# Optimization experiments

Hardware: AMD Instinct MI355X
Metric: run time of the kernel (lower is better)

The kernel has to match this reference:

```python
import jax, jax.numpy as jnp
import numpy as np
import math

H = 10  # hidden_dim (hardcoded in source)
D = 2   # data_dim (hardcoded in source)
T = 256
B = 2048

PARAM_SHAPES = {
    'fi_in_W': (D, H), 'fi_in_b': (H,), 'fi_h_W': (H, H), 'fi_h_b': (H,),
    'fi_mu_W': (H, H), 'fi_mu_b': (H,), 'fi_sg_W': (H, H), 'fi_sg_b': (H,),
    'inf_in_W': (D, H), 'inf_in_b': (H,), 'inf_j_W': (2 * H, H), 'inf_j_b': (H,),
    'inf_h_W': (H, H), 'inf_h_b': (H,), 'inf_mu_W': (H, H), 'inf_mu_b': (H,),
    'inf_sg_W': (H, H), 'inf_sg_b': (H,),
    'tr_h_W': (H, H), 'tr_h_b': (H,), 'tr_mu_W': (H, H), 'tr_mu_b': (H,),
    'tr_sg_W': (H, H), 'tr_sg_b': (H,),
    'gen_h1_W': (H, H), 'gen_h1_b': (H,), 'gen_h2_W': (H, H), 'gen_h2_b': (H,),
    'gen_mu_W': (H, D), 'gen_mu_b': (D,), 'gen_sg_W': (H, D), 'gen_sg_b': (D,),
}


def setup_inputs() -> dict:
    key = jax.random.key(0)
    names = list(PARAM_SHAPES)
    keys = jax.random.split(key, len(names) + 2)
    inp = {}
    inp['sequence'] = jax.random.normal(keys[0], (T, B, D), jnp.float32)
    inp['noise'] = jax.random.normal(keys[1], (T, B, H), jnp.float32)
    for n, k in zip(names, keys[2:]):
        inp[n] = 0.1 * jax.random.normal(k, PARAM_SHAPES[n], jnp.float32)
    # Transition sigma is tanh(.); shift its bias so sigma stays strictly positive
    # (a trained model would do the same; negative sigma makes the source's log(prod) NaN).
    inp['tr_sg_b'] = inp['tr_sg_b'] + 2.0
    return inp


def _forward(sequence, noise,
             fi_in_W, fi_in_b, fi_h_W, fi_h_b, fi_mu_W, fi_mu_b, fi_sg_W, fi_sg_b,
             inf_in_W, inf_in_b, inf_j_W, inf_j_b, inf_h_W, inf_h_b, inf_mu_W, inf_mu_b, inf_sg_W, inf_sg_b,
             tr_h_W, tr_h_b, tr_mu_W, tr_mu_b, tr_sg_W, tr_sg_b,
             gen_h1_W, gen_h1_b, gen_h2_W, gen_h2_b, gen_mu_W, gen_mu_b, gen_sg_W, gen_sg_b):

    def first_inf(x):
        h = jnp.tanh(x @ fi_in_W + fi_in_b)
        h = jnp.tanh(h @ fi_h_W + fi_h_b)
        return jnp.tanh(h @ fi_mu_W + fi_mu_b), jax.nn.sigmoid(h @ fi_sg_W + fi_sg_b) + 0.001

    def inference(x, z):
        e = jnp.tanh(x @ inf_in_W + inf_in_b)
        h = jnp.tanh(jnp.concatenate([e, z], -1) @ inf_j_W + inf_j_b)
        h = jnp.tanh(h @ inf_h_W + inf_h_b)
        return jnp.tanh(h @ inf_mu_W + inf_mu_b), jax.nn.sigmoid(h @ inf_sg_W + inf_sg_b) + 0.001

    def transition(z):
        h = jnp.tanh(z @ tr_h_W + tr_h_b)
        return jnp.tanh(h @ tr_mu_W + tr_mu_b), jnp.tanh(h @ tr_sg_W + tr_sg_b)

    def generator(z):
        h = jax.nn.relu(z @ gen_h1_W + gen_h1_b)
        h = jax.nn.relu(h @ gen_h2_W + gen_h2_b)
        return jax.nn.sigmoid(h @ gen_mu_W + gen_mu_b), jax.nn.sigmoid(h @ gen_sg_W + gen_sg_b)

    def kld(mu_q, sg_q, mu_p, sg_p):  # source GaussianKLD (treats sigma as variance)
        a = jnp.log(jnp.prod(sg_p, -1) / jnp.prod(sg_q, -1))
        b = jnp.sum(sg_q / sg_p, -1)
        c = jnp.sum((mu_p - mu_q) ** 2 / sg_p, -1)
        return 0.5 * (a + b + c - mu_q.shape[-1])

    def gll(mu, sg, target):  # source GaussianLL (note: log(pi), not 2*pi — faithful)
        a = jnp.log(jnp.prod(sg, -1))
        b = jnp.sum((target - mu) ** 2 / sg, -1)
        c = mu.shape[-1] * math.log(math.pi)
        return -0.5 * (a + b + c)

    # t = 0: first_inference against unit-Gaussian prior
    q_mu0, q_sg0 = first_inf(sequence[0])
    kl0 = kld(q_mu0, q_sg0, jnp.zeros_like(q_mu0), jnp.ones_like(q_sg0))
    z1 = q_mu0 + q_sg0 * noise[0]
    g_mu0, g_sg0 = generator(z1)
    loss0 = kl0 + gll(g_mu0, g_sg0, sequence[0])  # [B]

    def step(z_prev, xe):
        x_t, eps = xe
        pr_mu, pr_sg = transition(z_prev)
        q_mu, q_sg = inference(x_t, z_prev)
        kl_t = kld(q_mu, q_sg, pr_mu, pr_sg)
        z = q_mu + q_sg * eps
        m, s = generator(z)
        ll_t = gll(m, s, x_t)
        return z, (m, kl_t + ll_t)

    _, (gens_rest, step_losses) = jax.lax.scan(step, z1, (sequence[1:], noise[1:]))
    generations = jnp.concatenate([g_mu0[None], gens_rest], 0)  # [T, B, D]
    loss = loss0 + jnp.sum(step_losses, 0)                       # [B]
    return generations, -loss / sequence.shape[0]


def reference(sequence, noise,
              fi_in_W, fi_in_b, fi_h_W, fi_h_b, fi_mu_W, fi_mu_b, fi_sg_W, fi_sg_b,
              inf_in_W, inf_in_b, inf_j_W, inf_j_b, inf_h_W, inf_h_b, inf_mu_W, inf_mu_b, inf_sg_W, inf_sg_b,
              tr_h_W, tr_h_b, tr_mu_W, tr_mu_b, tr_sg_W, tr_sg_b,
              gen_h1_W, gen_h1_b, gen_h2_W, gen_h2_b, gen_mu_W, gen_mu_b, gen_sg_W, gen_sg_b):
    return _forward(sequence, noise,
                    fi_in_W, fi_in_b, fi_h_W, fi_h_b, fi_mu_W, fi_mu_b, fi_sg_W, fi_sg_b,
                    inf_in_W, inf_in_b, inf_j_W, inf_j_b, inf_h_W, inf_h_b, inf_mu_W, inf_mu_b, inf_sg_W, inf_sg_b,
                    tr_h_W, tr_h_b, tr_mu_W, tr_mu_b, tr_sg_W, tr_sg_b,
                    gen_h1_W, gen_h1_b, gen_h2_W, gen_h2_b, gen_mu_W, gen_mu_b, gen_sg_W, gen_sg_b)
```

## Files before the change

### kernel.cpp

```cpp
#include <hip/hip_runtime.h>
#include <math.h>

#define T_STEPS 256
#define BATCH   2048
#define HID     10

#define ZOFF   0
#define QMUOFF (T_STEPS*BATCH*HID)
#define QSGOFF (2*T_STEPS*BATCH*HID)
#define KLOFF  (3*T_STEPS*BATCH*HID)
#define LLOFF  (KLOFF + T_STEPS*BATCH)

#define S2P  2.8853900817779268f
#define SNP -1.4426950408889634f

typedef float v2f __attribute__((ext_vector_type(2)));

__device__ __forceinline__ float frcp(float x){ return __builtin_amdgcn_rcpf(x); }
__device__ __forceinline__ float ex2 (float x){ return __builtin_amdgcn_exp2f(x); }
__device__ __forceinline__ float ftanh2(float y){ return 1.f - 2.f*frcp(1.f + ex2(y)); }
__device__ __forceinline__ float fsigm2(float y){ return frcp(1.f + ex2(y)); }
__device__ __forceinline__ float ftanhU(float x){ return ftanh2(S2P*x); }
__device__ __forceinline__ float fsigmU(float x){ return fsigm2(SNP*x); }

template<int K> __device__ __forceinline__ float rotk(float x){
  return __int_as_float(__builtin_amdgcn_update_dpp(
      0, __float_as_int(x), 0x120 + K, 0xF, 0xF, false));
}
#define ROT16(r, v) do{ float _v=(v); r[0]=_v; \
  r[1]=rotk<1>(_v);  r[2]=rotk<2>(_v);  r[3]=rotk<3>(_v);  r[4]=rotk<4>(_v);  \
  r[5]=rotk<5>(_v);  r[6]=rotk<6>(_v);  r[7]=rotk<7>(_v);  r[8]=rotk<8>(_v);  \
  r[9]=rotk<9>(_v);  r[10]=rotk<10>(_v);r[11]=rotk<11>(_v);r[12]=rotk<12>(_v);\
  r[13]=rotk<13>(_v);r[14]=rotk<14>(_v);r[15]=rotk<15>(_v); }while(0)

#define ROTP(r, a, b) do{ float _a=(a), _b=(b); r[0]=(v2f){_a,_b}; \
  r[1]=(v2f){rotk<1>(_a),rotk<1>(_b)};   r[2]=(v2f){rotk<2>(_a),rotk<2>(_b)}; \
  r[3]=(v2f){rotk<3>(_a),rotk<3>(_b)};   r[4]=(v2f){rotk<4>(_a),rotk<4>(_b)}; \
  r[5]=(v2f){rotk<5>(_a),rotk<5>(_b)};   r[6]=(v2f){rotk<6>(_a),rotk<6>(_b)}; \
  r[7]=(v2f){rotk<7>(_a),rotk<7>(_b)};   r[8]=(v2f){rotk<8>(_a),rotk<8>(_b)}; \
  r[9]=(v2f){rotk<9>(_a),rotk<9>(_b)};   r[10]=(v2f){rotk<10>(_a),rotk<10>(_b)}; \
  r[11]=(v2f){rotk<11>(_a),rotk<11>(_b)};r[12]=(v2f){rotk<12>(_a),rotk<12>(_b)}; \
  r[13]=(v2f){rotk<13>(_a),rotk<13>(_b)};r[14]=(v2f){rotk<14>(_a),rotk<14>(_b)}; \
  r[15]=(v2f){rotk<15>(_a),rotk<15>(_b)}; }while(0)

__device__ __forceinline__ float dot16(const float* r, const float* w, float bias){
  float a0 = fmaf(r[0], w[0], bias);
  float a1 = r[1]*w[1];
  float a2 = r[2]*w[2];
  float a3 = r[3]*w[3];
  #pragma unroll
  for (int k=4;k<16;k+=4){
    a0 = fmaf(r[k  ], w[k  ], a0);
    a1 = fmaf(r[k+1], w[k+1], a1);
    a2 = fmaf(r[k+2], w[k+2], a2);
    a3 = fmaf(r[k+3], w[k+3], a3);
  }
  return (a0+a1)+(a2+a3);
}

__device__ __forceinline__ v2f dotp16(const v2f* r, const v2f* w, v2f init){
  v2f a0 = __builtin_elementwise_fma(r[0], w[0], init);
  v2f a1 = r[1]*w[1];
  v2f a2 = r[2]*w[2];
  v2f a3 = r[3]*w[3];
  #pragma unroll
  for (int k=4;k<16;k+=4){
    a0 = __builtin_elementwise_fma(r[k  ], w[k  ], a0);
    a1 = __builtin_elementwise_fma(r[k+1], w[k+1], a1);
    a2 = __builtin_elementwise_fma(r[k+2], w[k+2], a2);
    a3 = __builtin_elementwise_fma(r[k+3], w[k+3], a3);
  }
  return (a0+a1)+(a2+a3);
}

__device__ __forceinline__ float dot16x(const float* r, const v2f* w, float bias){
  float a0 = fmaf(r[0], w[0].x, bias);
  float a1 = r[1]*w[1].x;
  float a2 = r[2]*w[2].x;
  float a3 = r[3]*w[3].x;
  #pragma unroll
  for (int k=4;k<16;k+=4){
    a0 = fmaf(r[k  ], w[k  ].x, a0);
    a1 = fmaf(r[k+1], w[k+1].x, a1);
    a2 = fmaf(r[k+2], w[k+2].x, a2);
    a3 = fmaf(r[k+3], w[k+3].x, a3);
  }
  return (a0+a1)+(a2+a3);
}

template<int NROW, int NCOL>
__device__ __forceinline__ void loadrot(float* dst, const float* W, int j, int col,
                                        bool colok, float scale){
  int colc = colok ? col : 0;
  #pragma unroll
  for (int k=0;k<16;k++){
    int i = (j - k) & 15;
    bool v = colok && (i < NROW);
    int ic = v ? i : 0;
    float w = W[ic*NCOL + colc];
    dst[k] = v ? scale*w : 0.f;
  }
}
__device__ __forceinline__ float bload(const float* p, int idx, bool ok, float scale){
  float t = p[ok ? idx : 0];
  return ok ? scale*t : 0.f;
}
template<int X> __device__ __forceinline__ float xor16(float x){
  return __int_as_float(__builtin_amdgcn_ds_swizzle(__float_as_int(x), (X<<10)|0x1f));
}

struct P34 { const float* p[34]; float* ws; float* out; };

__global__ __attribute__((amdgpu_flat_work_group_size(64, 64), amdgpu_waves_per_eu(1, 1)))
void k1_recur(P34 prm)
{
  const int tid = threadIdx.x;
  const int j   = tid & 15;
  const int grp = tid >> 4;
  const int b   = blockIdx.x*4 + grp;
  const bool act = (j < HID);
  const int  jl  = act ? j : 0;

  const float* __restrict__ seq   = prm.p[0];
  const float* __restrict__ noise = prm.p[1];
  float* __restrict__ ws = prm.ws;

  float w_ii0   = bload(prm.p[10],      jl, act, S2P);
  float w_ii1   = bload(prm.p[10], 10 + jl, act, S2P);
  float b_in_in = bload(prm.p[11], jl, act, S2P);
  float tje[16], tjz[16], tmu[16], tsg[16], w_h[16];
  loadrot<10,10>(tje, prm.p[12],       j, j, act, S2P);
  loadrot<10,10>(tjz, prm.p[12] + 100, j, j, act, S2P);
  loadrot<10,10>(w_h, prm.p[14],       j, j, act, S2P);
  loadrot<10,10>(tmu, prm.p[16],       j, j, act, S2P);
  loadrot<10,10>(tsg, prm.p[18],       j, j, act, SNP);
  v2f wez[16], wmsg[16];
  #pragma unroll
  for (int k=0;k<16;k++){ wez[k]=(v2f){tje[k],tjz[k]}; wmsg[k]=(v2f){tmu[k],tsg[k]}; }
  float b_in_j  = bload(prm.p[13], jl, act, S2P);
  float b_in_h  = bload(prm.p[15], jl, act, S2P);
  float b_in_mu = bload(prm.p[17], jl, act, S2P);
  float b_in_sg = bload(prm.p[19], jl, act, SNP);
  const v2f bmsg = (v2f){b_in_mu, b_in_sg};

  auto ldx = [&](int t){ return *reinterpret_cast<const float2*>(seq + t*BATCH*2 + b*2); };
  auto lde = [&](int t){ return noise[t*BATCH*HID + b*HID + jl]; };

  float z_prev;
  float ae_c;

  {
    float w0 = bload(prm.p[2],      jl, act, S2P);
    float w1 = bload(prm.p[2], 10 + jl, act, S2P);
    float bb = bload(prm.p[3], jl, act, S2P);
    float f_h[16], f_mu[16], f_sg[16];
    loadrot<10,10>(f_h,  prm.p[4], j, j, act, S2P);  float fb_h  = bload(prm.p[5], jl, act, S2P);
    loadrot<10,10>(f_mu, prm.p[6], j, j, act, S2P);  float fb_mu = bload(prm.p[7], jl, act, S2P);
    loadrot<10,10>(f_sg, prm.p[8], j, j, act, SNP);  float fb_sg = bload(prm.p[9], jl, act, SNP);
    float2 x = ldx(0);
    float eps = lde(0);
    float h0 = ftanh2(fmaf(x.x, w0, fmaf(x.y, w1, bb)));
    float r0[16]; ROT16(r0, h0);
    float h1 = ftanh2(dot16(r0, f_h, fb_h));
    float r1[16]; ROT16(r1, h1);
    float mu = ftanh2(dot16(r1, f_mu, fb_mu));
    float sg = fsigm2(dot16(r1, f_sg, fb_sg)) + 0.001f;
    float term = act ? (sg + mu*mu - __logf(sg)) : 0.f;
    term += xor16<1>(term); term += xor16<2>(term); term += xor16<4>(term); term += xor16<8>(term);
    if (j == 0) ws[KLOFF + b] = 0.5f*term;
    float z = fmaf(sg, eps, mu);
    if (act){
      ws[ZOFF   + b*HID + jl] = z;
      ws[QMUOFF + b*HID + jl] = mu;
      ws[QSGOFF + b*HID + jl] = sg;
    }
    z_prev = z;
  }

  {
    float2 x1 = ldx(1);
    float e1 = ftanh2(fmaf(x1.x, w_ii0, fmaf(x1.y, w_ii1, b_in_in)));
    float re1[16]; ROT16(re1, e1);
    ae_c = dot16x(re1, wez, b_in_j);
  }

  auto step = [&](int t, float2 xa, float ec){
    float e = ftanh2(fmaf(xa.x, w_ii0, fmaf(xa.y, w_ii1, b_in_in)));
    v2f rez[16]; ROTP(rez, e, z_prev);
    v2f d1 = dotp16(rez, wez, (v2f){b_in_j, 0.f});
    float hj = ftanh2(ae_c + d1.y);
    float rhj[16]; ROT16(rhj, hj);
    float hi = ftanh2(dot16(rhj, w_h, b_in_h));
    float rhi[16]; ROT16(rhi, hi);
    v2f hh[16];
    #pragma unroll
    for (int k=0;k<16;k++) hh[k] = (v2f){rhi[k], rhi[k]};
    v2f d2 = dotp16(hh, wmsg, bmsg);
    float q_mu = ftanh2(d2.x);
    float q_sg = fsigm2(d2.y) + 0.001f;
    float z = fmaf(q_sg, ec, q_mu);
    int zW = (t*BATCH + b)*HID + jl;
    if (act){
      ws[ZOFF   + zW] = z;
      ws[QMUOFF + zW] = q_mu;
      ws[QSGOFF + zW] = q_sg;
    }
    z_prev = z;
    ae_c = d1.x;
  };

  float2 xq0=ldx(2), xq1=ldx(3), xq2=ldx(4), xq3=ldx(5);
  float  eq0=lde(1), eq1=lde(2), eq2=lde(3), eq3=lde(4);

  for (int bt = 0; bt < 62; ++bt){
    const int base = 4*bt;
    float2 xn0=ldx(base+6), xn1=ldx(base+7), xn2=ldx(base+8), xn3=ldx(base+9);
    float  en0=lde(base+5), en1=lde(base+6), en2=lde(base+7), en3=lde(base+8);
    step(base+1, xq0, eq0);
    step(base+2, xq1, eq1);
    step(base+3, xq2, eq2);
    step(base+4, xq3, eq3);
    xq0=xn0; xq1=xn1; xq2=xn2; xq3=xn3;
    eq0=en0; eq1=en1; eq2=en2; eq3=en3;
  }
  step(249, xq0, eq0);
  step(250, xq1, eq1);
  step(251, xq2, eq2);
  step(252, xq3, eq3);
  float2 xA=ldx(254), xB=ldx(255);
  float  eA=lde(253), eB=lde(254), eC=lde(255);
  step(253, xA, eA);
  step(254, xB, eB);
  step(255, xB, eC);
}

__global__ __attribute__((amdgpu_flat_work_group_size(256, 256), amdgpu_waves_per_eu(1, 1)))
void k2_gen(P34 prm)
{
  const int i = blockIdx.x*256 + threadIdx.x;
  float* __restrict__ ws = prm.ws;
  const float* __restrict__ seq = prm.p[0];
  float* __restrict__ out = prm.out;

  float w1[100], b1[10], w2[100], b2[10], wm[20], bm[2], wsg[20], bs[2];
  #pragma unroll
  for (int k=0;k<100;k++) w1[k] = prm.p[26][k];
  #pragma unroll
  for (int k=0;k<10;k++)  b1[k] = prm.p[27][k];
  #pragma unroll
  for (int k=0;k<100;k++) w2[k] = prm.p[28][k];
  #pragma unroll
  for (int k=0;k<10;k++)  b2[k] = prm.p[29][k];
  #pragma unroll
  for (int k=0;k<20;k++)  wm[k] = prm.p[30][k];
  #pragma unroll
  for (int k=0;k<2;k++)   bm[k] = prm.p[31][k];
  #pragma unroll
  for (int k=0;k<20;k++)  wsg[k]= prm.p[32][k];
  #pragma unroll
  for (int k=0;k<2;k++)   bs[k] = prm.p[33][k];

  const float* zp = ws + ZOFF + i*10;
  float z[10];
  #pragma unroll
  for (int k=0;k<5;k++){ float2 v = *reinterpret_cast<const float2*>(zp + 2*k); z[2*k]=v.x; z[2*k+1]=v.y; }

  float h1[10];
  #pragma unroll
  for (int o=0;o<10;o++){
    float a = b1[o];
    #pragma unroll
    for (int k=0;k<10;k++) a = fmaf(z[k], w1[k*10+o], a);
    h1[o] = fmaxf(a, 0.f);
  }
  float h2[10];
  #pragma unroll
  for (int o=0;o<10;o++){
    float a = b2[o];
    #pragma unroll
    for (int k=0;k<10;k++) a = fmaf(h1[k], w2[k*10+o], a);
    h2[o] = fmaxf(a, 0.f);
  }
  float m0,m1,s0,s1;
  {
    float am0=bm[0], am1=bm[1], as0=bs[0], as1=bs[1];
    #pragma unroll
    for (int k=0;k<10;k++){
      am0 = fmaf(h2[k], wm[k*2+0], am0);
      am1 = fmaf(h2[k], wm[k*2+1], am1);
      as0 = fmaf(h2[k], wsg[k*2+0], as0);
      as1 = fmaf(h2[k], wsg[k*2+1], as1);
    }
    m0=fsigmU(am0); m1=fsigmU(am1); s0=fsigmU(as0); s1=fsigmU(as1);
  }
  float2 xv = *reinterpret_cast<const float2*>(seq + i*2);
  float d0 = xv.x - m0, d1 = xv.y - m1;
  float ll = __logf(s0) + __logf(s1) + d0*d0*frcp(s0) + d1*d1*frcp(s1);
  float2 mo; mo.x = m0; mo.y = m1;
  *reinterpret_cast<float2*>(out + i*2) = mo;
  ws[LLOFF + i] = -0.5f*ll;
}

__global__ __attribute__((amdgpu_flat_work_group_size(256, 256), amdgpu_waves_per_eu(1, 1)))
void k2_kl(P34 prm)
{
  const int i = blockIdx.x*256 + threadIdx.x;
  const int t = 1 + (i >> 11);
  const int b = i & (BATCH-1);
  float* __restrict__ ws = prm.ws;

  float wh[100], bh[10], wmu[100], bmu[10], wsg[100], bsg[10];
  #pragma unroll
  for (int k=0;k<100;k++) wh[k]  = prm.p[20][k];
  #pragma unroll
  for (int k=0;k<10;k++)  bh[k]  = prm.p[21][k];
  #pragma unroll
  for (int k=0;k<100;k++) wmu[k] = prm.p[22][k];
  #pragma unroll
  for (int k=0;k<10;k++)  bmu[k] = prm.p[23][k];
  #pragma unroll
  for (int k=0;k<100;k++) wsg[k] = prm.p[24][k];
  #pragma unroll
  for (int k=0;k<10;k++)  bsg[k] = prm.p[25][k];

  const float* zp  = ws + ZOFF   + ((t-1)*BATCH + b)*10;
  const float* qmp = ws + QMUOFF + (t*BATCH + b)*10;
  const float* qsp = ws + QSGOFF + (t*BATCH + b)*10;
  float z[10], qmu[10], qsg[10];
  #pragma unroll
  for (int k=0;k<5;k++){
    float2 v;
    v = *reinterpret_cast<const float2*>(zp  + 2*k); z[2*k]=v.x;   z[2*k+1]=v.y;
    v = *reinterpret_cast<const float2*>(qmp + 2*k); qmu[2*k]=v.x; qmu[2*k+1]=v.y;
    v = *reinterpret_cast<const float2*>(qsp + 2*k); qsg[2*k]=v.x; qsg[2*k+1]=v.y;
  }

  float th[10];
  #pragma unroll
  for (int o=0;o<10;o++){
    float a = bh[o];
    #pragma unroll
    for (int k=0;k<10;k++) a = fmaf(z[k], wh[k*10+o], a);
    th[o] = ftanhU(a);
  }
  float kl = 0.f;
  #pragma unroll
  for (int o=0;o<10;o++){
    float am = bmu[o], as = bsg[o];
    #pragma unroll
    for (int k=0;k<10;k++){
      am = fmaf(th[k], wmu[k*10+o], am);
      as = fmaf(th[k], wsg[k*10+o], as);
    }
    float prmu = ftanhU(am);
    float prsg = ftanhU(as);
    float dmu = prmu - qmu[o];
    float rp  = frcp(prsg);
    kl += __logf(prsg*frcp(qsg[o])) + (qsg[o] + dmu*dmu)*rp;
  }
  ws[KLOFF + t*BATCH + b] = 0.5f*kl;
}

__global__ __launch_bounds__(256, 1) void k3_loss(P34 prm)
{
  __shared__ float red[256];
  const int tid = threadIdx.x;
  const int bl  = tid & 63;
  const int q   = tid >> 6;
  const int b   = blockIdx.x*64 + bl;
  const float* __restrict__ kl = prm.ws + KLOFF;
  const float* __restrict__ ll = prm.ws + LLOFF;
  float s = 0.f;
  #pragma unroll 4
  for (int tt = 0; tt < 64; ++tt){
    int t = q*64 + tt;
    s += kl[t*BATCH + b] + ll[t*BATCH + b];
  }
  red[tid] = s;
  __syncthreads();
  if (q == 0){
    s = red[bl] + red[bl+64] + red[bl+128] + red[bl+192];
    const float LOGPI = 1.1447298858494002f;
    prm.out[T_STEPS*BATCH*2 + b] = -s*(1.0f/(float)T_STEPS) + 5.0f + LOGPI;
  }
}

extern "C" void kernel_launch(void* const* d_in, const int* in_sizes, int n_in,
                              void* d_out, int out_size, void* d_ws, size_t ws_size,
                              hipStream_t stream) {
  P34 prm;
  for (int i = 0; i < 34; ++i) prm.p[i] = (const float*)d_in[i];
  prm.ws  = (float*)d_ws;
  prm.out = (float*)d_out;
  hipLaunchKernelGGL(k1_recur, dim3(512),  dim3(64),  0, stream, prm);
  hipLaunchKernelGGL(k2_gen,   dim3(2048), dim3(256), 0, stream, prm);
  hipLaunchKernelGGL(k2_kl,    dim3(2040), dim3(256), 0, stream, prm);
  hipLaunchKernelGGL(k3_loss,  dim3(32),   dim3(256), 0, stream, prm);
}
```

Baseline: 173.8 us.

## Fuse generator, transition KL and loss reduction into the recurrent kernel

Folds the generator MLP, the transition prior KL term and the per-batch loss sum into the sequential recurrence kernel. Each step now evaluates these with the same DPP-rotated lane-per-hidden-unit dot products and accumulates the loss in registers, so the z/q_mu/q_sg workspace writes and the three follow-up kernels go away. The trade-off is that the serial 256-step recurrence on only 512 small blocks now carries extra arithmetic per step. That lengthens the critical path, where before the same work ran as highly parallel separate kernels.

```diff
diff --git a/kernel.cpp b/kernel.cpp
--- a/kernel.cpp
+++ b/kernel.cpp
@@ -5,14 +5,10 @@
 #define BATCH   2048
 #define HID     10
 
-#define ZOFF   0
-#define QMUOFF (T_STEPS*BATCH*HID)
-#define QSGOFF (2*T_STEPS*BATCH*HID)
-#define KLOFF  (3*T_STEPS*BATCH*HID)
-#define LLOFF  (KLOFF + T_STEPS*BATCH)
-
 #define S2P  2.8853900817779268f
 #define SNP -1.4426950408889634f
+#define LN2  0.6931471805599453f
+#define LOGPI 1.1447298858494002f
 
 typedef float v2f __attribute__((ext_vector_type(2)));
 
@@ -20,8 +16,6 @@
 __device__ __forceinline__ float ex2 (float x){ return __builtin_amdgcn_exp2f(x); }
 __device__ __forceinline__ float ftanh2(float y){ return 1.f - 2.f*frcp(1.f + ex2(y)); }
 __device__ __forceinline__ float fsigm2(float y){ return frcp(1.f + ex2(y)); }
-__device__ __forceinline__ float ftanhU(float x){ return ftanh2(S2P*x); }
-__device__ __forceinline__ float fsigmU(float x){ return fsigm2(SNP*x); }
 
 template<int K> __device__ __forceinline__ float rotk(float x){
   return __int_as_float(__builtin_amdgcn_update_dpp(
@@ -57,7 +51,6 @@
   }
   return (a0+a1)+(a2+a3);
 }
-
 __device__ __forceinline__ v2f dotp16(const v2f* r, const v2f* w, v2f init){
   v2f a0 = __builtin_elementwise_fma(r[0], w[0], init);
   v2f a1 = r[1]*w[1];
@@ -72,7 +65,6 @@
   }
   return (a0+a1)+(a2+a3);
 }
-
 __device__ __forceinline__ float dot16x(const float* r, const v2f* w, float bias){
   float a0 = fmaf(r[0], w[0].x, bias);
   float a1 = r[1]*w[1].x;
@@ -84,6 +76,20 @@
     a1 = fmaf(r[k+1], w[k+1].x, a1);
     a2 = fmaf(r[k+2], w[k+2].x, a2);
     a3 = fmaf(r[k+3], w[k+3].x, a3);
+  }
+  return (a0+a1)+(a2+a3);
+}
+__device__ __forceinline__ float dot16y(const v2f* r, const float* w, float bias){
+  float a0 = fmaf(r[0].y, w[0], bias);
+  float a1 = r[1].y*w[1];
+  float a2 = r[2].y*w[2];
+  float a3 = r[3].y*w[3];
+  #pragma unroll
+  for (int k=4;k<16;k+=4){
+    a0 = fmaf(r[k  ].y, w[k  ], a0);
+    a1 = fmaf(r[k+1].y, w[k+1], a1);
+    a2 = fmaf(r[k+2].y, w[k+2], a2);
+    a3 = fmaf(r[k+3].y, w[k+3], a3);
   }
   return (a0+a1)+(a2+a3);
 }
@@ -112,7 +118,7 @@
 struct P34 { const float* p[34]; float* ws; float* out; };
 
 __global__ __attribute__((amdgpu_flat_work_group_size(64, 64), amdgpu_waves_per_eu(1, 1)))
-void k1_recur(P34 prm)
+void k1_fused(P34 prm)
 {
   const int tid = threadIdx.x;
   const int j   = tid & 15;
@@ -123,7 +129,7 @@
 
   const float* __restrict__ seq   = prm.p[0];
   const float* __restrict__ noise = prm.p[1];
-  float* __restrict__ ws = prm.ws;
+  float* __restrict__ out = prm.out;
 
   float w_ii0   = bload(prm.p[10],      jl, act, S2P);
   float w_ii1   = bload(prm.p[10], 10 + jl, act, S2P);
@@ -143,11 +149,31 @@
   float b_in_sg = bload(prm.p[19], jl, act, SNP);
   const v2f bmsg = (v2f){b_in_mu, b_in_sg};
 
+  float wth[16];  loadrot<10,10>(wth,  prm.p[20], j, j, act, S2P);
+  float bth  = bload(prm.p[21], jl, act, S2P);
+  float wtmu[16]; loadrot<10,10>(wtmu, prm.p[22], j, j, act, S2P);
+  float btmu = bload(prm.p[23], jl, act, S2P);
+  float wtsg[16]; loadrot<10,10>(wtsg, prm.p[24], j, j, act, S2P);
+  float btsg = bload(prm.p[25], jl, act, S2P);
+
+  float wg1[16]; loadrot<10,10>(wg1, prm.p[26], j, j, act, 1.f);
+  float bg1 = bload(prm.p[27], jl, act, 1.f);
+  float wg2[16]; loadrot<10,10>(wg2, prm.p[28], j, j, act, 1.f);
+  float bg2 = bload(prm.p[29], jl, act, 1.f);
+  const bool isd = (j < 4);
+  const float* Wgo = (j < 2) ? prm.p[30] : prm.p[32];
+  const float* Bgo = (j < 2) ? prm.p[31] : prm.p[33];
+  float wgo[16]; loadrot<10,2>(wgo, Wgo, j, j & 1, isd, SNP);
+  float bgo = bload(Bgo, j & 1, isd, SNP);
+
+  float LL = 0.f;
+  float L2 = 0.f;
+
   auto ldx = [&](int t){ return *reinterpret_cast<const float2*>(seq + t*BATCH*2 + b*2); };
   auto lde = [&](int t){ return noise[t*BATCH*HID + b*HID + jl]; };
 
-  float z_prev;
-  float ae_c;
+  float z_prev, ae_c;
+  float2 x0v, x1v;
 
   {
     float w0 = bload(prm.p[2],      jl, act, S2P);
@@ -157,37 +183,57 @@
     loadrot<10,10>(f_h,  prm.p[4], j, j, act, S2P);  float fb_h  = bload(prm.p[5], jl, act, S2P);
     loadrot<10,10>(f_mu, prm.p[6], j, j, act, S2P);  float fb_mu = bload(prm.p[7], jl, act, S2P);
     loadrot<10,10>(f_sg, prm.p[8], j, j, act, SNP);  float fb_sg = bload(prm.p[9], jl, act, SNP);
-    float2 x = ldx(0);
+    x0v = ldx(0);
     float eps = lde(0);
-    float h0 = ftanh2(fmaf(x.x, w0, fmaf(x.y, w1, bb)));
+    float h0 = ftanh2(fmaf(x0v.x, w0, fmaf(x0v.y, w1, bb)));
     float r0[16]; ROT16(r0, h0);
     float h1 = ftanh2(dot16(r0, f_h, fb_h));
     float r1[16]; ROT16(r1, h1);
     float mu = ftanh2(dot16(r1, f_mu, fb_mu));
     float sg = fsigm2(dot16(r1, f_sg, fb_sg)) + 0.001f;
-    float term = act ? (sg + mu*mu - __logf(sg)) : 0.f;
-    term += xor16<1>(term); term += xor16<2>(term); term += xor16<4>(term); term += xor16<8>(term);
-    if (j == 0) ws[KLOFF + b] = 0.5f*term;
-    float z = fmaf(sg, eps, mu);
     if (act){
-      ws[ZOFF   + b*HID + jl] = z;
-      ws[QMUOFF + b*HID + jl] = mu;
-      ws[QSGOFF + b*HID + jl] = sg;
+      LL += sg + mu*mu;
+      L2 -= __log2f(sg);
     }
-    z_prev = z;
+    z_prev = fmaf(sg, eps, mu);
   }
 
   {
-    float2 x1 = ldx(1);
-    float e1 = ftanh2(fmaf(x1.x, w_ii0, fmaf(x1.y, w_ii1, b_in_in)));
+    x1v = ldx(1);
+    float e1 = ftanh2(fmaf(x1v.x, w_ii0, fmaf(x1v.y, w_ii1, b_in_in)));
     float re1[16]; ROT16(re1, e1);
-    ae_c = dot16x(re1, wez, b_in_j);
-  }
-
-  auto step = [&](int t, float2 xa, float ec){
+    v2f wtmp[16];
+    #pragma unroll
+    for (int k=0;k<16;k++) wtmp[k]=wez[k];
+    ae_c = dot16x(re1, wtmp, b_in_j);
+  }
+
+  auto step = [&](int t, float2 xa, float ec, float2 xll){
     float e = ftanh2(fmaf(xa.x, w_ii0, fmaf(xa.y, w_ii1, b_in_in)));
     v2f rez[16]; ROTP(rez, e, z_prev);
     v2f d1 = dotp16(rez, wez, (v2f){b_in_j, 0.f});
+
+    float g1 = fmaxf(dot16y(rez, wg1, bg1), 0.f);
+    float rg1[16]; ROT16(rg1, g1);
+    float g2 = fmaxf(dot16(rg1, wg2, bg2), 0.f);
+    float rg2[16]; ROT16(rg2, g2);
+    float ygo = dot16(rg2, wgo, bgo);
+    float tgo = 1.f + ex2(ygo);
+    float tpl = rotk<14>(tgo);
+    if (j < 2){
+      float m = frcp(tgo);
+      out[(t-1)*(BATCH*2) + b*2 + j] = m;
+      float xd = (j==0) ? xll.x : xll.y;
+      float dd = xd - m;
+      LL -= dd*dd*tpl;
+      L2 += __log2f(tpl);
+    }
+
+    float th = ftanh2(dot16y(rez, wth, bth));
+    float rth[16]; ROT16(rth, th);
+    float prmu = ftanh2(dot16(rth, wtmu, btmu));
+    float prsg = ftanh2(dot16(rth, wtsg, btsg));
+
     float hj = ftanh2(ae_c + d1.y);
     float rhj[16]; ROT16(rhj, hj);
     float hi = ftanh2(dot16(rhj, w_h, b_in_h));
@@ -199,11 +245,12 @@
     float q_mu = ftanh2(d2.x);
     float q_sg = fsigm2(d2.y) + 0.001f;
     float z = fmaf(q_sg, ec, q_mu);
-    int zW = (t*BATCH + b)*HID + jl;
+
     if (act){
-      ws[ZOFF   + zW] = z;
-      ws[QMUOFF + zW] = q_mu;
-      ws[QSGOFF + zW] = q_sg;
+      float dmu = prmu - q_mu;
+      float rp  = frcp(prsg);
+      LL += (q_sg + dmu*dmu)*rp;
+      L2 += __log2f(prsg) - __log2f(q_sg);
     }
     z_prev = z;
     ae_c = d1.x;
@@ -211,178 +258,53 @@
 
   float2 xq0=ldx(2), xq1=ldx(3), xq2=ldx(4), xq3=ldx(5);
   float  eq0=lde(1), eq1=lde(2), eq2=lde(3), eq3=lde(4);
+  float2 xc0=x0v, xc1=x1v;
 
   for (int bt = 0; bt < 62; ++bt){
     const int base = 4*bt;
     float2 xn0=ldx(base+6), xn1=ldx(base+7), xn2=ldx(base+8), xn3=ldx(base+9);
     float  en0=lde(base+5), en1=lde(base+6), en2=lde(base+7), en3=lde(base+8);
-    step(base+1, xq0, eq0);
-    step(base+2, xq1, eq1);
-    step(base+3, xq2, eq2);
-    step(base+4, xq3, eq3);
+    step(base+1, xq0, eq0, xc0);
+    step(base+2, xq1, eq1, xc1);
+    step(base+3, xq2, eq2, xq0);
+    step(base+4, xq3, eq3, xq1);
+    xc0=xq2; xc1=xq3;
     xq0=xn0; xq1=xn1; xq2=xn2; xq3=xn3;
     eq0=en0; eq1=en1; eq2=en2; eq3=en3;
   }
-  step(249, xq0, eq0);
-  step(250, xq1, eq1);
-  step(251, xq2, eq2);
-  step(252, xq3, eq3);
+  step(249, xq0, eq0, xc0);
+  step(250, xq1, eq1, xc1);
+  step(251, xq2, eq2, xq0);
+  step(252, xq3, eq3, xq1);
   float2 xA=ldx(254), xB=ldx(255);
   float  eA=lde(253), eB=lde(254), eC=lde(255);
-  step(253, xA, eA);
-  step(254, xB, eB);
-  step(255, xB, eC);
-}
-
-__global__ __attribute__((amdgpu_flat_work_group_size(256, 256), amdgpu_waves_per_eu(1, 1)))
-void k2_gen(P34 prm)
-{
-  const int i = blockIdx.x*256 + threadIdx.x;
-  float* __restrict__ ws = prm.ws;
-  const float* __restrict__ seq = prm.p[0];
-  float* __restrict__ out = prm.out;
-
-  float w1[100], b1[10], w2[100], b2[10], wm[20], bm[2], wsg[20], bs[2];
-  #pragma unroll
-  for (int k=0;k<100;k++) w1[k] = prm.p[26][k];
-  #pragma unroll
-  for (int k=0;k<10;k++)  b1[k] = prm.p[27][k];
-  #pragma unroll
-  for (int k=0;k<100;k++) w2[k] = prm.p[28][k];
-  #pragma unroll
-  for (int k=0;k<10;k++)  b2[k] = prm.p[29][k];
-  #pragma unroll
-  for (int k=0;k<20;k++)  wm[k] = prm.p[30][k];
-  #pragma unroll
-  for (int k=0;k<2;k++)   bm[k] = prm.p[31][k];
-  #pragma unroll
-  for (int k=0;k<20;k++)  wsg[k]= prm.p[32][k];
-  #pragma unroll
-  for (int k=0;k<2;k++)   bs[k] = prm.p[33][k];
-
-  const float* zp = ws + ZOFF + i*10;
-  float z[10];
-  #pragma unroll
-  for (int k=0;k<5;k++){ float2 v = *reinterpret_cast<const float2*>(zp + 2*k); z[2*k]=v.x; z[2*k+1]=v.y; }
-
-  float h1[10];
-  #pragma unroll
-  for (int o=0;o<10;o++){
-    float a = b1[o];
-    #pragma unroll
-    for (int k=0;k<10;k++) a = fmaf(z[k], w1[k*10+o], a);
-    h1[o] = fmaxf(a, 0.f);
-  }
-  float h2[10];
-  #pragma unroll
-  for (int o=0;o<10;o++){
-    float a = b2[o];
-    #pragma unroll
-    for (int k=0;k<10;k++) a = fmaf(h1[k], w2[k*10+o], a);
-    h2[o] = fmaxf(a, 0.f);
-  }
-  float m0,m1,s0,s1;
+  step(253, xA, eA, xq2);
+  step(254, xB, eB, xq3);
+  step(255, xB, eC, xA);
+
   {
-    float am0=bm[0], am1=bm[1], as0=bs[0], as1=bs[1];
-    #pragma unroll
-    for (int k=0;k<10;k++){
-      am0 = fmaf(h2[k], wm[k*2+0], am0);
-      am1 = fmaf(h2[k], wm[k*2+1], am1);
-      as0 = fmaf(h2[k], wsg[k*2+0], as0);
-      as1 = fmaf(h2[k], wsg[k*2+1], as1);
+    float rzf[16]; ROT16(rzf, z_prev);
+    float g1 = fmaxf(dot16(rzf, wg1, bg1), 0.f);
+    float rg1[16]; ROT16(rg1, g1);
+    float g2 = fmaxf(dot16(rg1, wg2, bg2), 0.f);
+    float rg2[16]; ROT16(rg2, g2);
+    float ygo = dot16(rg2, wgo, bgo);
+    float tgo = 1.f + ex2(ygo);
+    float tpl = rotk<14>(tgo);
+    if (j < 2){
+      float m = frcp(tgo);
+      out[255*(BATCH*2) + b*2 + j] = m;
+      float xd = (j==0) ? xB.x : xB.y;
+      float dd = xd - m;
+      LL -= dd*dd*tpl;
+      L2 += __log2f(tpl);
     }
-    m0=fsigmU(am0); m1=fsigmU(am1); s0=fsigmU(as0); s1=fsigmU(as1);
-  }
-  float2 xv = *reinterpret_cast<const float2*>(seq + i*2);
-  float d0 = xv.x - m0, d1 = xv.y - m1;
-  float ll = __logf(s0) + __logf(s1) + d0*d0*frcp(s0) + d1*d1*frcp(s1);
-  float2 mo; mo.x = m0; mo.y = m1;
-  *reinterpret_cast<float2*>(out + i*2) = mo;
-  ws[LLOFF + i] = -0.5f*ll;
-}
-
-__global__ __attribute__((amdgpu_flat_work_group_size(256, 256), amdgpu_waves_per_eu(1, 1)))
-void k2_kl(P34 prm)
-{
-  const int i = blockIdx.x*256 + threadIdx.x;
-  const int t = 1 + (i >> 11);
-  const int b = i & (BATCH-1);
-  float* __restrict__ ws = prm.ws;
-
-  float wh[100], bh[10], wmu[100], bmu[10], wsg[100], bsg[10];
-  #pragma unroll
-  for (int k=0;k<100;k++) wh[k]  = prm.p[20][k];
-  #pragma unroll
-  for (int k=0;k<10;k++)  bh[k]  = prm.p[21][k];
-  #pragma unroll
-  for (int k=0;k<100;k++) wmu[k] = prm.p[22][k];
-  #pragma unroll
-  for (int k=0;k<10;k++)  bmu[k] = prm.p[23][k];
-  #pragma unroll
-  for (int k=0;k<100;k++) wsg[k] = prm.p[24][k];
-  #pragma unroll
-  for (int k=0;k<10;k++)  bsg[k] = prm.p[25][k];
-
-  const float* zp  = ws + ZOFF   + ((t-1)*BATCH + b)*10;
-  const float* qmp = ws + QMUOFF + (t*BATCH + b)*10;
-  const float* qsp = ws + QSGOFF + (t*BATCH + b)*10;
-  float z[10], qmu[10], qsg[10];
-  #pragma unroll
-  for (int k=0;k<5;k++){
-    float2 v;
-    v = *reinterpret_cast<const float2*>(zp  + 2*k); z[2*k]=v.x;   z[2*k+1]=v.y;
-    v = *reinterpret_cast<const float2*>(qmp + 2*k); qmu[2*k]=v.x; qmu[2*k+1]=v.y;
-    v = *reinterpret_cast<const float2*>(qsp + 2*k); qsg[2*k]=v.x; qsg[2*k+1]=v.y;
-  }
-
-  float th[10];
-  #pragma unroll
-  for (int o=0;o<10;o++){
-    float a = bh[o];
-    #pragma unroll
-    for (int k=0;k<10;k++) a = fmaf(z[k], wh[k*10+o], a);
-    th[o] = ftanhU(a);
-  }
-  float kl = 0.f;
-  #pragma unroll
-  for (int o=0;o<10;o++){
-    float am = bmu[o], as = bsg[o];
-    #pragma unroll
-    for (int k=0;k<10;k++){
-      am = fmaf(th[k], wmu[k*10+o], am);
-      as = fmaf(th[k], wsg[k*10+o], as);
-    }
-    float prmu = ftanhU(am);
-    float prsg = ftanhU(as);
-    float dmu = prmu - qmu[o];
-    float rp  = frcp(prsg);
-    kl += __logf(prsg*frcp(qsg[o])) + (qsg[o] + dmu*dmu)*rp;
-  }
-  ws[KLOFF + t*BATCH + b] = 0.5f*kl;
-}
-
-__global__ __launch_bounds__(256, 1) void k3_loss(P34 prm)
-{
-  __shared__ float red[256];
-  const int tid = threadIdx.x;
-  const int bl  = tid & 63;
-  const int q   = tid >> 6;
-  const int b   = blockIdx.x*64 + bl;
-  const float* __restrict__ kl = prm.ws + KLOFF;
-  const float* __restrict__ ll = prm.ws + LLOFF;
-  float s = 0.f;
-  #pragma unroll 4
-  for (int tt = 0; tt < 64; ++tt){
-    int t = q*64 + tt;
-    s += kl[t*BATCH + b] + ll[t*BATCH + b];
-  }
-  red[tid] = s;
-  __syncthreads();
-  if (q == 0){
-    s = red[bl] + red[bl+64] + red[bl+128] + red[bl+192];
-    const float LOGPI = 1.1447298858494002f;
-    prm.out[T_STEPS*BATCH*2 + b] = -s*(1.0f/(float)T_STEPS) + 5.0f + LOGPI;
-  }
+  }
+
+  float tot = fmaf(LN2, L2, LL);
+  tot += xor16<1>(tot); tot += xor16<2>(tot); tot += xor16<4>(tot); tot += xor16<8>(tot);
+  if (j == 0)
+    out[T_STEPS*BATCH*2 + b] = -tot*(1.0f/512.0f) + 5.0f + LOGPI;
 }
 
 extern "C" void kernel_launch(void* const* d_in, const int* in_sizes, int n_in,
@@ -392,8 +314,5 @@
   for (int i = 0; i < 34; ++i) prm.p[i] = (const float*)d_in[i];
   prm.ws  = (float*)d_ws;
   prm.out = (float*)d_out;
-  hipLaunchKernelGGL(k1_recur, dim3(512),  dim3(64),  0, stream, prm);
-  hipLaunchKernelGGL(k2_gen,   dim3(2048), dim3(256), 0, stream, prm);
-  hipLaunchKernelGGL(k2_kl,    dim3(2040), dim3(256), 0, stream, prm);
-  hipLaunchKernelGGL(k3_loss,  dim3(32),   dim3(256), 0, stream, prm);
-}
+  hipLaunchKernelGGL(k1_fused, dim3(512), dim3(64), 0, stream, prm);
+}
```

Result: slower. 231.1 us (+33.0%).
